# Kernel optimization log

Measured on AMD Instinct MI355X. Metric: run time of the kernel, lower is better.

## Reference

```python
import jax, jax.numpy as jnp
import numpy as np

B, S, D_MODEL, D_HEAD = 4, 4096, 768, 64

def setup_inputs() -> dict:
    key = jax.random.key(0)
    kx, kq, kk, kv = jax.random.split(key, 4)
    scale = 1.0 / np.sqrt(D_MODEL)
    return {
        "x": jax.random.normal(kx, (B, S, D_MODEL), dtype=jnp.float32),
        "W_Q": jax.random.normal(kq, (D_MODEL, D_HEAD), dtype=jnp.float32) * scale,
        "W_K": jax.random.normal(kk, (D_MODEL, D_HEAD), dtype=jnp.float32) * scale,
        "W_V": jax.random.normal(kv, (D_MODEL, D_HEAD), dtype=jnp.float32) * scale,
    }

def reference(x, W_Q, W_K, W_V):
    # x: [B, S, d_model]; projections to [B, S, d_head]
    Q = x @ W_Q
    K = x @ W_K
    V = x @ W_V
    d_head = Q.shape[-1]
    # scores: [B, S, S], scaled dot product
    A = jnp.einsum('bid,bjd->bij', Q, K) / jnp.sqrt(jnp.asarray(d_head, Q.dtype))
    S_len = x.shape[1]
    causal = jnp.tril(jnp.ones((S_len, S_len), dtype=bool))
    A = jnp.where(causal[None, :, :], A, -jnp.inf)
    A = jax.nn.softmax(A, axis=-1)
    return jnp.einsum('bij,bjd->bid', A, V)
```

## Files before the change

### kernel.cpp

```cpp
#include <hip/hip_runtime.h>
#include <hip/hip_bf16.h>

typedef __bf16 bf16_t;
typedef bf16_t bf16x8 __attribute__((ext_vector_type(8)));
typedef float f32x4 __attribute__((ext_vector_type(4)));
typedef float f32x16 __attribute__((ext_vector_type(16)));
typedef unsigned int u32;

#define NB 4
#define SS 4096
#define DM 768
#define DH 64
#define NROW (NB * SS)
#define CSCALE (0.125f * 1.44269504088896341f)
#define MFIX 24.0f

#define QOFF 0u
#define KOFF 2097152u
#define VOFF 4194304u
#define WOFF 6291456u

#define SB() __builtin_amdgcn_sched_barrier(0)

__device__ __forceinline__ u32 cvtpk_bf16(float lo, float hi) {
    u32 r;
    asm volatile("v_cvt_pk_bf16_f32 %0, %1, %2" : "=v"(r) : "v"(lo), "v"(hi));
    return r;
}

__global__ __launch_bounds__(256) void wt_kernel(const float* __restrict__ wq,
                                                 const float* __restrict__ wk,
                                                 const float* __restrict__ wv,
                                                 bf16_t* __restrict__ wt) {
    int id = blockIdx.x * 256 + threadIdx.x;
    if (id >= 3 * DM * DH) return;
    int m = id / (DM * DH);
    int r = id - m * (DM * DH);
    int k = r >> 6;
    int c = r & 63;
    const float* w = (m == 0) ? wq : (m == 1) ? wk : wv;
    float v = w[k * DH + c];
    if (m == 0) v *= CSCALE;
    wt[(size_t)m * DH * DM + (size_t)c * DM + k] = (bf16_t)v;
}

__global__ __launch_bounds__(256, 3) void proj_kernel(const float* __restrict__ x,
                                                      const bf16_t* __restrict__ wt,
                                                      bf16_t* __restrict__ Qo,
                                                      bf16_t* __restrict__ Ko,
                                                      bf16_t* __restrict__ Vt) {
    __shared__ __align__(16) float xs[4][2048];

    const int tid = threadIdx.x;
    const int lane = tid & 63;
    const int wid = tid >> 6;
    const int l15 = lane & 15;
    const int g = lane >> 4;
    const int m0 = blockIdx.x * 32;

    const int srow0 = tid >> 4;
    const int skc0 = (tid & 15) ^ (srow0 & 7);
    const int srow1 = 16 + srow0;
    const int skc1 = (tid & 15) ^ (srow1 & 7);
    const float* sb0 = x + (size_t)(m0 + srow0) * DM + skc0 * 4;
    const float* sb1 = x + (size_t)(m0 + srow1) * DM + skc1 * 4;

    #define STAGE(bsel, t_) do {                                                    \
        __builtin_amdgcn_global_load_lds(                                           \
            (const __attribute__((address_space(1))) void*)(sb0 + (t_) * 64),       \
            (__attribute__((address_space(3))) void*)(&xs[bsel][wid * 256]),        \
            16, 0, 0);                                                              \
        __builtin_amdgcn_global_load_lds(                                           \
            (const __attribute__((address_space(1))) void*)(sb1 + (t_) * 64),       \
            (__attribute__((address_space(3))) void*)(&xs[bsel][1024 + wid * 256]), \
            16, 0, 0); } while (0)

    size_t wbase[3];
    #pragma unroll
    for (int n = 0; n < 3; n++) {
        const int gn = wid * 3 + n;
        const int mm = gn >> 2;
        const int cj = gn & 3;
        wbase[n] = (size_t)mm * DH * DM + (size_t)(cj * 16 + l15) * DM + g * 8;
    }

    f32x4 acc[2][3];
    #pragma unroll
    for (int fi = 0; fi < 2; fi++)
        #pragma unroll
        for (int n = 0; n < 3; n++)
            #pragma unroll
            for (int j = 0; j < 4; j++) acc[fi][n][j] = 0.0f;

    int roff[2][2];
    #pragma unroll
    for (int kk = 0; kk < 2; kk++)
        #pragma unroll
        for (int c = 0; c < 2; c++)
            roff[kk][c] = l15 * 64 + ((kk * 8 + g * 2 + c) ^ (l15 & 7)) * 4;

    bf16x8 wslot[3][3][2];

    #pragma unroll
    for (int n = 0; n < 3; n++)
        #pragma unroll
        for (int kk = 0; kk < 2; kk++)
            wslot[0][n][kk] = *reinterpret_cast<const bf16x8*>(wt + wbase[n] + kk * 32);
    SB();
    STAGE(0, 0); SB();
    #pragma unroll
    for (int n = 0; n < 3; n++)
        #pragma unroll
        for (int kk = 0; kk < 2; kk++)
            wslot[1][n][kk] = *reinterpret_cast<const bf16x8*>(wt + wbase[n] + 64 + kk * 32);
    SB();
    STAGE(1, 1); SB();
    STAGE(2, 2); SB();
    asm volatile("s_waitcnt vmcnt(10)");
    SB();
    __builtin_amdgcn_s_barrier();
    SB();

    #pragma unroll
    for (int t = 0; t < 12; t++) {
        if (t + 2 < 12) {
            #pragma unroll
            for (int n = 0; n < 3; n++)
                #pragma unroll
                for (int kk = 0; kk < 2; kk++)
                    wslot[(t + 2) % 3][n][kk] = *reinterpret_cast<const bf16x8*>(
                        wt + wbase[n] + (t + 2) * 64 + kk * 32);
        }
        SB();
        if (t + 3 < 12) { STAGE((t + 3) & 3, t + 3); }
        SB();
        bf16x8 a[2][2];
        #pragma unroll
        for (int fi = 0; fi < 2; fi++)
            #pragma unroll
            for (int kk = 0; kk < 2; kk++) {
                f32x4 c0 = *reinterpret_cast<const f32x4*>(&xs[t & 3][fi * 1024 + roff[kk][0]]);
                f32x4 c1 = *reinterpret_cast<const f32x4*>(&xs[t & 3][fi * 1024 + roff[kk][1]]);
                bf16x8 tt;
                #pragma unroll
                for (int j = 0; j < 4; j++) { tt[j] = (bf16_t)c0[j]; tt[4 + j] = (bf16_t)c1[j]; }
                a[fi][kk] = tt;
            }
        #pragma unroll
        for (int n = 0; n < 3; n++)
            #pragma unroll
            for (int kk = 0; kk < 2; kk++)
                #pragma unroll
                for (int fi = 0; fi < 2; fi++)
                    acc[fi][n] = __builtin_amdgcn_mfma_f32_16x16x32_bf16(
                        a[fi][kk], wslot[t % 3][n][kk], acc[fi][n], 0, 0, 0);

        if (t < 11) {
            if (t <= 8)       { asm volatile("s_waitcnt vmcnt(10)"); }
            else if (t == 9)  { asm volatile("s_waitcnt vmcnt(8)");  }
            else              { asm volatile("s_waitcnt vmcnt(0)");  }
            SB();
            __builtin_amdgcn_s_barrier();
            SB();
        }
    }
    #undef STAGE

    #pragma unroll
    for (int n = 0; n < 3; n++) {
        const int gn = wid * 3 + n;
        const int mm = gn >> 2;
        const int cj = gn & 3;
        #pragma unroll
        for (int fi = 0; fi < 2; fi++)
            #pragma unroll
            for (int j = 0; j < 4; j++) {
                int row = m0 + fi * 16 + g * 4 + j;
                int col = cj * 16 + l15;
                float v = acc[fi][n][j];
                if (mm == 0)      Qo[(size_t)row * DH + col] = (bf16_t)v;
                else if (mm == 1) Ko[(size_t)row * DH + col] = (bf16_t)v;
                else              Vt[(size_t)col * NROW + row] = (bf16_t)v;
            }
    }
}

__global__ __launch_bounds__(256, 2) void attn_kernel(const bf16_t* __restrict__ Q,
                                                      const bf16_t* __restrict__ K,
                                                      const bf16_t* __restrict__ Vt,
                                                      float* __restrict__ out) {
    __shared__ float Ob[2][2][16][64];
    __shared__ float Ls[2][64];

    const int tid = threadIdx.x;
    const int lane = tid & 63;
    const int w = tid >> 6;
    const int l31 = lane & 31;
    const int hi = lane >> 5;
    const int bx = blockIdx.x;
    const int b = (bx & 7) >> 1;
    const int r_ = (bx >> 3) * 2 + (bx & 1);
    const int tile = (r_ < 64) ? (127 - r_) : (r_ - 64);
    const int q0 = tile * 32;
    const int nkv = (tile >> 1) + 1;
    const int q = q0 + l31;

    const bf16_t* Qb = Q + (size_t)b * SS * DH;
    const bf16_t* Kb = K + (size_t)b * SS * DH;
    const bf16_t* Vb = Vt + (size_t)b * SS;

    bf16x8 bq[4];
    #pragma unroll
    for (int ks = 0; ks < 4; ks++)
        bq[ks] = *reinterpret_cast<const bf16x8*>(
            Qb + (size_t)(q0 + l31) * DH + ks * 16 + hi * 8);

    f32x16 o[2];
    #pragma unroll
    for (int c = 0; c < 2; c++)
        #pragma unroll
        for (int r = 0; r < 16; r++) o[c][r] = 0.0f;
    float lsum = 0.0f;

    for (int kt = w; kt < nkv; kt += 4) {
        const int kv0 = kt * 64;
        const bool diag = (kv0 + 63 > q0);

        bf16x8 ak0[4];
        #pragma unroll
        for (int ks = 0; ks < 4; ks++)
            ak0[ks] = *reinterpret_cast<const bf16x8*>(
                Kb + (size_t)(kv0 + l31) * DH + ks * 16 + hi * 8);
        SB();
        bf16x8 ak1[4];
        #pragma unroll
        for (int ks = 0; ks < 4; ks++)
            ak1[ks] = *reinterpret_cast<const bf16x8*>(
                Kb + (size_t)(kv0 + 32 + l31) * DH + ks * 16 + hi * 8);
        SB();
        bf16x8 vf[2][4];
        #pragma unroll
        for (int c = 0; c < 2; c++)
            #pragma unroll
            for (int kks = 0; kks < 4; kks++)
                vf[c][kks] = *reinterpret_cast<const bf16x8*>(
                    Vb + (size_t)(c * 32 + l31) * NROW + kv0 + kks * 16 + hi * 8);
        SB();

        u32 pa[4][4];
        f32x16 s0;
        #pragma unroll
        for (int r = 0; r < 16; r++) s0[r] = 0.0f;
        #pragma unroll
        for (int ks = 0; ks < 4; ks++)
            s0 = __builtin_amdgcn_mfma_f32_32x32x16_bf16(ak0[ks], bq[ks], s0, 0, 0, 0);
        f32x16 s1;
        #pragma unroll
        for (int r = 0; r < 16; r++) s1[r] = 0.0f;
        #pragma unroll
        for (int ks = 0; ks < 4; ks++)
            s1 = __builtin_amdgcn_mfma_f32_32x32x16_bf16(ak1[ks], bq[ks], s1, 0, 0, 0);

        #pragma unroll
        for (int blk = 0; blk < 2; blk++) {
            const f32x16& s = blk ? s1 : s0;
            const int kvbase = kv0 + blk * 32 + 4 * hi;
            float p[16];
            #pragma unroll
            for (int r = 0; r < 16; r++) {
                float e = exp2f(s[r] - MFIX);
                if (diag) {
                    int kv = kvbase + (r & 3) + 8 * (r >> 2);
                    e = (kv > q) ? 0.0f : e;
                }
                p[r] = e;
                lsum += e;
            }
            #pragma unroll
            for (int ks2 = 0; ks2 < 2; ks2++) {
                u32 w01 = cvtpk_bf16(p[8 * ks2 + 0], p[8 * ks2 + 1]);
                u32 w23 = cvtpk_bf16(p[8 * ks2 + 2], p[8 * ks2 + 3]);
                u32 w45 = cvtpk_bf16(p[8 * ks2 + 4], p[8 * ks2 + 5]);
                u32 w67 = cvtpk_bf16(p[8 * ks2 + 6], p[8 * ks2 + 7]);
                asm volatile("v_permlane32_swap_b32 %0, %1" : "+v"(w01), "+v"(w45));
                asm volatile("v_permlane32_swap_b32 %0, %1" : "+v"(w23), "+v"(w67));
                pa[blk * 2 + ks2][0] = w01;
                pa[blk * 2 + ks2][1] = w23;
                pa[blk * 2 + ks2][2] = w45;
                pa[blk * 2 + ks2][3] = w67;
            }
        }

        #pragma unroll
        for (int kks = 0; kks < 4; kks++) {
            union { u32 w4[4]; bf16x8 v; } uu;
            uu.w4[0] = pa[kks][0];
            uu.w4[1] = pa[kks][1];
            uu.w4[2] = pa[kks][2];
            uu.w4[3] = pa[kks][3];
            #pragma unroll
            for (int c = 0; c < 2; c++)
                o[c] = __builtin_amdgcn_mfma_f32_32x32x16_bf16(uu.v, vf[c][kks], o[c], 0, 0, 0);
        }
    }

    if (w >= 2) {
        #pragma unroll
        for (int c = 0; c < 2; c++)
            #pragma unroll
            for (int r = 0; r < 16; r++) Ob[w - 2][c][r][lane] = o[c][r];
        Ls[w - 2][lane] = lsum;
    }
    __syncthreads();
    if (w < 2) {
        #pragma unroll
        for (int c = 0; c < 2; c++)
            #pragma unroll
            for (int r = 0; r < 16; r++) o[c][r] += Ob[w][c][r][lane];
        lsum += Ls[w][lane];
    }
    __syncthreads();
    if (w == 1) {
        #pragma unroll
        for (int c = 0; c < 2; c++)
            #pragma unroll
            for (int r = 0; r < 16; r++) Ob[0][c][r][lane] = o[c][r];
        Ls[0][lane] = lsum;
    }
    __syncthreads();
    if (w == 0) {
        #pragma unroll
        for (int c = 0; c < 2; c++)
            #pragma unroll
            for (int r = 0; r < 16; r++) o[c][r] += Ob[0][c][r][lane];
        lsum += Ls[0][lane];

        float lfull = lsum + __shfl_xor(lsum, 32);
        float* ob = out + ((size_t)b * SS + q0) * DH;
        #pragma unroll
        for (int c = 0; c < 2; c++)
            #pragma unroll
            for (int r = 0; r < 16; r++) {
                const int qr = (r & 3) + 8 * (r >> 2) + 4 * hi;
                float lr = __shfl(lfull, qr);
                ob[(size_t)qr * DH + c * 32 + l31] = o[c][r] / lr;
            }
    }
}

extern "C" void kernel_launch(void* const* d_in, const int* in_sizes, int n_in,
                              void* d_out, int out_size, void* d_ws, size_t ws_size,
                              hipStream_t stream) {
    const float* x  = (const float*)d_in[0];
    const float* wq = (const float*)d_in[1];
    const float* wk = (const float*)d_in[2];
    const float* wv = (const float*)d_in[3];
    float* out = (float*)d_out;

    char* ws = (char*)d_ws;
    bf16_t* Qw = (bf16_t*)(ws + QOFF);
    bf16_t* Kw = (bf16_t*)(ws + KOFF);
    bf16_t* Vt = (bf16_t*)(ws + VOFF);
    bf16_t* Wt = (bf16_t*)(ws + WOFF);

    hipLaunchKernelGGL(wt_kernel, dim3((3 * DM * DH + 255) / 256), dim3(256), 0, stream,
                       wq, wk, wv, Wt);
    hipLaunchKernelGGL(proj_kernel, dim3(NROW / 32), dim3(256), 0, stream,
                       x, Wt, Qw, Kw, Vt);
    hipLaunchKernelGGL(attn_kernel, dim3(NB * 128), dim3(256), 0, stream,
                       Qw, Kw, Vt, out);
}
```

Before: 66.96 us.

## Split KV range of each query tile across two blocks with atomic-flag merge

Doubles the attention grid so each query tile's KV blocks are split between two workgroups (split-K style). Each half writes its partial O and row sums to a workspace buffer, and the second block to finish, detected with an atomicAdd counter, merges both halves and writes the normalized output. This raises parallelism and evens out load across the 256 CUs for causal tiles. In exchange it adds partial-buffer traffic, thread fences, a memset launch and an extra merge step.

```diff
diff --git a/kernel.cpp b/kernel.cpp
--- a/kernel.cpp
+++ b/kernel.cpp
@@ -19,6 +19,10 @@
 #define KOFF 2097152u
 #define VOFF 4194304u
 #define WOFF 6291456u
+#define FOFF 6586368u
+#define POFF 6590464u
+#define PART_F32 2112
+#define WS_NEED (POFF + 1024ull * 8448ull)
 
 #define SB() __builtin_amdgcn_sched_barrier(0)
 
@@ -188,7 +192,9 @@
 __global__ __launch_bounds__(256, 2) void attn_kernel(const bf16_t* __restrict__ Q,
                                                       const bf16_t* __restrict__ K,
                                                       const bf16_t* __restrict__ Vt,
-                                                      float* __restrict__ out) {
+                                                      float* __restrict__ out,
+                                                      float* __restrict__ part,
+                                                      int* __restrict__ flags) {
     __shared__ float Ob[2][2][16][64];
     __shared__ float Ls[2][64];
 
@@ -198,8 +204,9 @@
     const int l31 = lane & 31;
     const int hi = lane >> 5;
     const int bx = blockIdx.x;
-    const int b = (bx & 7) >> 1;
-    const int r_ = (bx >> 3) * 2 + (bx & 1);
+    const int b = bx & 3;
+    const int h = (bx >> 2) & 1;
+    const int r_ = bx >> 3;
     const int tile = (r_ < 64) ? (127 - r_) : (r_ - 64);
     const int q0 = tile * 32;
     const int nkv = (tile >> 1) + 1;
@@ -222,7 +229,7 @@
         for (int r = 0; r < 16; r++) o[c][r] = 0.0f;
     float lsum = 0.0f;
 
-    for (int kt = w; kt < nkv; kt += 4) {
+    for (int kt = h * 4 + w; kt < nkv; kt += 8) {
         const int kv0 = kt * 64;
         const bool diag = (kv0 + 63 > q0);
 
@@ -328,24 +335,45 @@
         Ls[0][lane] = lsum;
     }
     __syncthreads();
-    if (w == 0) {
-        #pragma unroll
-        for (int c = 0; c < 2; c++)
-            #pragma unroll
-            for (int r = 0; r < 16; r++) o[c][r] += Ob[0][c][r][lane];
-        lsum += Ls[0][lane];
-
-        float lfull = lsum + __shfl_xor(lsum, 32);
-        float* ob = out + ((size_t)b * SS + q0) * DH;
-        #pragma unroll
-        for (int c = 0; c < 2; c++)
-            #pragma unroll
-            for (int r = 0; r < 16; r++) {
-                const int qr = (r & 3) + 8 * (r >> 2) + 4 * hi;
-                float lr = __shfl(lfull, qr);
-                ob[(size_t)qr * DH + c * 32 + l31] = o[c][r] / lr;
-            }
-    }
+    if (w != 0) return;
+
+    #pragma unroll
+    for (int c = 0; c < 2; c++)
+        #pragma unroll
+        for (int r = 0; r < 16; r++) o[c][r] += Ob[0][c][r][lane];
+    lsum += Ls[0][lane];
+
+    const int fid = b * 128 + tile;
+    const int pid = fid * 2 + h;
+    float* P = part + (size_t)pid * PART_F32;
+    #pragma unroll
+    for (int c = 0; c < 2; c++)
+        #pragma unroll
+        for (int r = 0; r < 16; r++) P[(c * 16 + r) * 64 + lane] = o[c][r];
+    P[2048 + lane] = lsum;
+    __threadfence();
+    int old = 0;
+    if (lane == 0) old = atomicAdd(&flags[fid], 1);
+    old = __shfl(old, 0);
+    if (old == 0) return;
+    __threadfence();
+    const float* Po = part + (size_t)(pid ^ 1) * PART_F32;
+    #pragma unroll
+    for (int c = 0; c < 2; c++)
+        #pragma unroll
+        for (int r = 0; r < 16; r++) o[c][r] += Po[(c * 16 + r) * 64 + lane];
+    lsum += Po[2048 + lane];
+
+    float lfull = lsum + __shfl_xor(lsum, 32);
+    float* ob = out + ((size_t)b * SS + q0) * DH;
+    #pragma unroll
+    for (int c = 0; c < 2; c++)
+        #pragma unroll
+        for (int r = 0; r < 16; r++) {
+            const int qr = (r & 3) + 8 * (r >> 2) + 4 * hi;
+            float lr = __shfl(lfull, qr);
+            ob[(size_t)qr * DH + c * 32 + l31] = o[c][r] / lr;
+        }
 }
 
 extern "C" void kernel_launch(void* const* d_in, const int* in_sizes, int n_in,
@@ -362,11 +390,15 @@
     bf16_t* Kw = (bf16_t*)(ws + KOFF);
     bf16_t* Vt = (bf16_t*)(ws + VOFF);
     bf16_t* Wt = (bf16_t*)(ws + WOFF);
+    int*    flags = (int*)(ws + FOFF);
+    float*  part  = (float*)(ws + POFF);
 
     hipLaunchKernelGGL(wt_kernel, dim3((3 * DM * DH + 255) / 256), dim3(256), 0, stream,
                        wq, wk, wv, Wt);
     hipLaunchKernelGGL(proj_kernel, dim3(NROW / 32), dim3(256), 0, stream,
                        x, Wt, Qw, Kw, Vt);
-    hipLaunchKernelGGL(attn_kernel, dim3(NB * 128), dim3(256), 0, stream,
-                       Qw, Kw, Vt, out);
+
+    hipMemsetAsync(flags, 0, 512 * sizeof(int), stream);
+    hipLaunchKernelGGL(attn_kernel, dim3(NB * 128 * 2), dim3(256), 0, stream,
+                       Qw, Kw, Vt, out, part, flags);
 }
```

Result: slower. 120.8 us (+80.4%).

## Split causal attention KV range across two blocks and merge partials

Applied to the files above, without the earlier changes.

Each query tile's KV loop is now split across two blocks, each taking interleaved 64-wide KV tiles, which doubles the grid to 1024 blocks. The fixed-max exp2 trick makes the partial sums additive, so each block writes unnormalized O and the row sums to a workspace buffer. A new merge kernel adds the two partials and divides by the total. This aims to improve occupancy and load balance over the wide spread of causal tile lengths, at the cost of an extra launch and partial-sum traffic. The old single-pass kernel is kept as a fallback when the workspace is too small.

```diff
diff --git a/kernel.cpp b/kernel.cpp
--- a/kernel.cpp
+++ b/kernel.cpp
@@ -19,6 +19,9 @@
 #define KOFF 2097152u
 #define VOFF 4194304u
 #define WOFF 6291456u
+#define POFF 6586368u
+#define PART_F32 2112
+#define WS_NEED (POFF + 1024ull * PART_F32 * 4ull)
 
 #define SB() __builtin_amdgcn_sched_barrier(0)
 
@@ -185,10 +188,198 @@
     }
 }
 
-__global__ __launch_bounds__(256, 2) void attn_kernel(const bf16_t* __restrict__ Q,
-                                                      const bf16_t* __restrict__ K,
-                                                      const bf16_t* __restrict__ Vt,
-                                                      float* __restrict__ out) {
+__global__ __launch_bounds__(256, 2) void attn_split(const bf16_t* __restrict__ Q,
+                                                     const bf16_t* __restrict__ K,
+                                                     const bf16_t* __restrict__ Vt,
+                                                     float* __restrict__ part) {
+    __shared__ float Ob[2][2][16][64];
+    __shared__ float Ls[2][64];
+
+    const int tid = threadIdx.x;
+    const int lane = tid & 63;
+    const int w = tid >> 6;
+    const int l31 = lane & 31;
+    const int hi = lane >> 5;
+    const int bx = blockIdx.x;
+    const int b = bx & 3;
+    const int h = (bx >> 2) & 1;
+    const int r_ = bx >> 3;
+    const int tile = (r_ < 64) ? (127 - r_) : (r_ - 64);
+    const int q0 = tile * 32;
+    const int nkv = (tile >> 1) + 1;
+    const int q = q0 + l31;
+
+    const bf16_t* Qb = Q + (size_t)b * SS * DH;
+    const bf16_t* Kb = K + (size_t)b * SS * DH;
+    const bf16_t* Vb = Vt + (size_t)b * SS;
+
+    bf16x8 bq[4];
+    #pragma unroll
+    for (int ks = 0; ks < 4; ks++)
+        bq[ks] = *reinterpret_cast<const bf16x8*>(
+            Qb + (size_t)(q0 + l31) * DH + ks * 16 + hi * 8);
+
+    f32x16 o[2];
+    #pragma unroll
+    for (int c = 0; c < 2; c++)
+        #pragma unroll
+        for (int r = 0; r < 16; r++) o[c][r] = 0.0f;
+    float lsum = 0.0f;
+
+    for (int kt = h * 4 + w; kt < nkv; kt += 8) {
+        const int kv0 = kt * 64;
+        const bool diag = (kv0 + 63 > q0);
+
+        bf16x8 ak0[4];
+        #pragma unroll
+        for (int ks = 0; ks < 4; ks++)
+            ak0[ks] = *reinterpret_cast<const bf16x8*>(
+                Kb + (size_t)(kv0 + l31) * DH + ks * 16 + hi * 8);
+        SB();
+        bf16x8 ak1[4];
+        #pragma unroll
+        for (int ks = 0; ks < 4; ks++)
+            ak1[ks] = *reinterpret_cast<const bf16x8*>(
+                Kb + (size_t)(kv0 + 32 + l31) * DH + ks * 16 + hi * 8);
+        SB();
+        bf16x8 vf[2][4];
+        #pragma unroll
+        for (int c = 0; c < 2; c++)
+            #pragma unroll
+            for (int kks = 0; kks < 4; kks++)
+                vf[c][kks] = *reinterpret_cast<const bf16x8*>(
+                    Vb + (size_t)(c * 32 + l31) * NROW + kv0 + kks * 16 + hi * 8);
+        SB();
+
+        u32 pa[4][4];
+        f32x16 s0;
+        #pragma unroll
+        for (int r = 0; r < 16; r++) s0[r] = 0.0f;
+        #pragma unroll
+        for (int ks = 0; ks < 4; ks++)
+            s0 = __builtin_amdgcn_mfma_f32_32x32x16_bf16(ak0[ks], bq[ks], s0, 0, 0, 0);
+        f32x16 s1;
+        #pragma unroll
+        for (int r = 0; r < 16; r++) s1[r] = 0.0f;
+        #pragma unroll
+        for (int ks = 0; ks < 4; ks++)
+            s1 = __builtin_amdgcn_mfma_f32_32x32x16_bf16(ak1[ks], bq[ks], s1, 0, 0, 0);
+
+        #pragma unroll
+        for (int blk = 0; blk < 2; blk++) {
+            const f32x16& s = blk ? s1 : s0;
+            const int kvbase = kv0 + blk * 32 + 4 * hi;
+            float p[16];
+            #pragma unroll
+            for (int r = 0; r < 16; r++) {
+                float e = exp2f(s[r] - MFIX);
+                if (diag) {
+                    int kv = kvbase + (r & 3) + 8 * (r >> 2);
+                    e = (kv > q) ? 0.0f : e;
+                }
+                p[r] = e;
+                lsum += e;
+            }
+            #pragma unroll
+            for (int ks2 = 0; ks2 < 2; ks2++) {
+                u32 w01 = cvtpk_bf16(p[8 * ks2 + 0], p[8 * ks2 + 1]);
+                u32 w23 = cvtpk_bf16(p[8 * ks2 + 2], p[8 * ks2 + 3]);
+                u32 w45 = cvtpk_bf16(p[8 * ks2 + 4], p[8 * ks2 + 5]);
+                u32 w67 = cvtpk_bf16(p[8 * ks2 + 6], p[8 * ks2 + 7]);
+                asm volatile("v_permlane32_swap_b32 %0, %1" : "+v"(w01), "+v"(w45));
+                asm volatile("v_permlane32_swap_b32 %0, %1" : "+v"(w23), "+v"(w67));
+                pa[blk * 2 + ks2][0] = w01;
+                pa[blk * 2 + ks2][1] = w23;
+                pa[blk * 2 + ks2][2] = w45;
+                pa[blk * 2 + ks2][3] = w67;
+            }
+        }
+
+        #pragma unroll
+        for (int kks = 0; kks < 4; kks++) {
+            union { u32 w4[4]; bf16x8 v; } uu;
+            uu.w4[0] = pa[kks][0];
+            uu.w4[1] = pa[kks][1];
+            uu.w4[2] = pa[kks][2];
+            uu.w4[3] = pa[kks][3];
+            #pragma unroll
+            for (int c = 0; c < 2; c++)
+                o[c] = __builtin_amdgcn_mfma_f32_32x32x16_bf16(uu.v, vf[c][kks], o[c], 0, 0, 0);
+        }
+    }
+
+    if (w >= 2) {
+        #pragma unroll
+        for (int c = 0; c < 2; c++)
+            #pragma unroll
+            for (int r = 0; r < 16; r++) Ob[w - 2][c][r][lane] = o[c][r];
+        Ls[w - 2][lane] = lsum;
+    }
+    __syncthreads();
+    if (w < 2) {
+        #pragma unroll
+        for (int c = 0; c < 2; c++)
+            #pragma unroll
+            for (int r = 0; r < 16; r++) o[c][r] += Ob[w][c][r][lane];
+        lsum += Ls[w][lane];
+    }
+    __syncthreads();
+    if (w == 1) {
+        #pragma unroll
+        for (int c = 0; c < 2; c++)
+            #pragma unroll
+            for (int r = 0; r < 16; r++) Ob[0][c][r][lane] = o[c][r];
+        Ls[0][lane] = lsum;
+    }
+    __syncthreads();
+    if (w != 0) return;
+
+    #pragma unroll
+    for (int c = 0; c < 2; c++)
+        #pragma unroll
+        for (int r = 0; r < 16; r++) o[c][r] += Ob[0][c][r][lane];
+    lsum += Ls[0][lane];
+
+    float* P = part + (size_t)(((b * 128 + tile) << 1) + h) * PART_F32;
+    #pragma unroll
+    for (int c = 0; c < 2; c++)
+        #pragma unroll
+        for (int r = 0; r < 16; r++) P[(c * 16 + r) * 64 + lane] = o[c][r];
+    P[2048 + lane] = lsum;
+}
+
+__global__ __launch_bounds__(256) void merge_kernel(const float* __restrict__ part,
+                                                    float* __restrict__ out) {
+    const int gw = blockIdx.x * 4 + (threadIdx.x >> 6);
+    const int lane = threadIdx.x & 63;
+    const int l31 = lane & 31;
+    const int hi = lane >> 5;
+    const int b = gw >> 7;
+    const int tile = gw & 127;
+    const int q0 = tile * 32;
+
+    const float* PA = part + (size_t)((b * 128 + tile) << 1) * PART_F32;
+    const float* PB = PA + PART_F32;
+
+    float lsum = PA[2048 + lane] + PB[2048 + lane];
+    float lfull = lsum + __shfl_xor(lsum, 32);
+
+    float* ob = out + ((size_t)b * SS + q0) * DH;
+    #pragma unroll
+    for (int c = 0; c < 2; c++)
+        #pragma unroll
+        for (int r = 0; r < 16; r++) {
+            float v = PA[(c * 16 + r) * 64 + lane] + PB[(c * 16 + r) * 64 + lane];
+            const int qr = (r & 3) + 8 * (r >> 2) + 4 * hi;
+            float lr = __shfl(lfull, qr);
+            ob[(size_t)qr * DH + c * 32 + l31] = v / lr;
+        }
+}
+
+__global__ __launch_bounds__(256, 2) void attn_mono(const bf16_t* __restrict__ Q,
+                                                    const bf16_t* __restrict__ K,
+                                                    const bf16_t* __restrict__ Vt,
+                                                    float* __restrict__ out) {
     __shared__ float Ob[2][2][16][64];
     __shared__ float Ls[2][64];
 
@@ -362,11 +553,20 @@
     bf16_t* Kw = (bf16_t*)(ws + KOFF);
     bf16_t* Vt = (bf16_t*)(ws + VOFF);
     bf16_t* Wt = (bf16_t*)(ws + WOFF);
+    float*  part = (float*)(ws + POFF);
 
     hipLaunchKernelGGL(wt_kernel, dim3((3 * DM * DH + 255) / 256), dim3(256), 0, stream,
                        wq, wk, wv, Wt);
     hipLaunchKernelGGL(proj_kernel, dim3(NROW / 32), dim3(256), 0, stream,
                        x, Wt, Qw, Kw, Vt);
-    hipLaunchKernelGGL(attn_kernel, dim3(NB * 128), dim3(256), 0, stream,
-                       Qw, Kw, Vt, out);
-}
+
+    if (ws_size >= WS_NEED) {
+        hipLaunchKernelGGL(attn_split, dim3(NB * 128 * 2), dim3(256), 0, stream,
+                           Qw, Kw, Vt, part);
+        hipLaunchKernelGGL(merge_kernel, dim3(128), dim3(256), 0, stream,
+                           part, out);
+    } else {
+        hipLaunchKernelGGL(attn_mono, dim3(NB * 128), dim3(256), 0, stream,
+                           Qw, Kw, Vt, out);
+    }
+}
```

Result: slower. 89.12 us (+33.1%).
